# Performance work log

Measured on AMD Instinct MI355X. Metric: run time of the kernel, lower is better.

The kernel has to match this reference:

```python
import jax, jax.numpy as jnp
import numpy as np

B, TE, TD, D = 8, 2048, 2048, 256

def setup_inputs() -> dict:
    key = jax.random.key(0)
    k1, k2 = jax.random.split(key)
    encoder_outputs = jax.random.normal(k1, (B, TE, D), dtype=jnp.float32)
    decoder_outputs = jax.random.normal(k2, (B, TD, D), dtype=jnp.float32)
    return {"encoder_outputs": encoder_outputs, "decoder_outputs": decoder_outputs}

def reference(encoder_outputs, decoder_outputs):
    # luong_score[b,e,t] = sum_d enc[b,e,d] * dec[b,t,d]   (batch_dot with dec transposed)
    luong_score = jnp.einsum('bed,btd->bet', encoder_outputs, decoder_outputs)
    # softmax over encoder-time axis (axis=1)
    luong_score = jax.nn.softmax(luong_score, axis=1)
    # original does expand_dims + broadcast-multiply + sum over axis=1;
    # same math as a contraction over e: context[b,t,d] = sum_e score[b,e,t]*enc[b,e,d]
    encoder_vector = jnp.einsum('bet,bed->btd', luong_score, encoder_outputs)
    return jnp.concatenate([decoder_outputs, encoder_vector], axis=-1)
```

## Files before the change

kernel.cpp:

```cpp
#include <hip/hip_runtime.h>

typedef _Float16 f16;
typedef _Float16 f16x4 __attribute__((ext_vector_type(4)));
typedef _Float16 f16x8 __attribute__((ext_vector_type(8)));
typedef float    f32x4 __attribute__((ext_vector_type(4)));

#define NB   8
#define TE   2048
#define TD   2048
#define DIM  256
#define NSPLIT 4
#define LOG2E 1.44269504088896340736f

#define AS1(p) ((const __attribute__((address_space(1))) void*)(p))
#define AS3(p) ((__attribute__((address_space(3))) void*)(p))

__global__ __launch_bounds__(256) void prep_kernel(const float* __restrict__ enc,
                                                   f16* __restrict__ ench,
                                                   f16* __restrict__ enct) {
    __shared__ f16 tile[64][72];
    int b  = blockIdx.z;
    int e0 = blockIdx.x * 64;
    int d0 = blockIdx.y * 64;
    int tid = threadIdx.x;
    {
        int e  = tid >> 2;
        int dg = (tid & 3) * 16;
        const float* p = enc + ((size_t)b * TE + e0 + e) * DIM + d0 + dg;
        float4 v0 = *(const float4*)(p);
        float4 v1 = *(const float4*)(p + 4);
        float4 v2 = *(const float4*)(p + 8);
        float4 v3 = *(const float4*)(p + 12);
        f16x8 o0, o1;
        o0[0]=(f16)v0.x; o0[1]=(f16)v0.y; o0[2]=(f16)v0.z; o0[3]=(f16)v0.w;
        o0[4]=(f16)v1.x; o0[5]=(f16)v1.y; o0[6]=(f16)v1.z; o0[7]=(f16)v1.w;
        o1[0]=(f16)v2.x; o1[1]=(f16)v2.y; o1[2]=(f16)v2.z; o1[3]=(f16)v2.w;
        o1[4]=(f16)v3.x; o1[5]=(f16)v3.y; o1[6]=(f16)v3.z; o1[7]=(f16)v3.w;
        *(f16x8*)&tile[e][dg]     = o0;
        *(f16x8*)&tile[e][dg + 8] = o1;
        f16* hp = ench + ((size_t)b * TE + e0 + e) * DIM + d0 + dg;
        *(f16x8*)(hp)     = o0;
        *(f16x8*)(hp + 8) = o1;
    }
    __syncthreads();
    {
        int d  = tid >> 2;
        int eg = (tid & 3) * 16;
        f16x8 o0, o1;
        #pragma unroll
        for (int ii = 0; ii < 8; ii++) o0[ii] = tile[eg + ii][d];
        #pragma unroll
        for (int ii = 0; ii < 8; ii++) o1[ii] = tile[eg + 8 + ii][d];
        f16* qp = enct + ((size_t)b * DIM + d0 + d) * TE + e0 + eg;
        *(f16x8*)(qp)     = o0;
        *(f16x8*)(qp + 8) = o1;
    }
}

#define LDS_NAT0 0
#define LDS_NAT1 16384
#define LDS_TR   32768
#define LDS_P    49152

__global__ __launch_bounds__(256, 2) void attn_kernel(
        const float* __restrict__ dec32,
        const f16*  __restrict__ enc_h,
        const f16*  __restrict__ enc_t,
        float* __restrict__ out,
        f16*   __restrict__ ctxp,
        float* __restrict__ m_arr,
        float* __restrict__ l_arr,
        int nsplit) {
    __shared__ char lds[54272];
    const int tid  = threadIdx.x;
    const int lane = tid & 63;
    const int wave = tid >> 6;
    const int th   = wave >> 1;
    const int dh   = wave & 1;
    const int tcol = lane & 15;
    const int q    = lane >> 4;

    int xb, b, z;
    if (nsplit == NSPLIT) {
        int fid = blockIdx.x + 32 * (blockIdx.y + 8 * blockIdx.z);
        int c = fid & 7, j = fid >> 3;
        int p = c * 4 + (j >> 5);
        xb = j & 31; b = p & 7; z = p >> 3;
    } else { xb = blockIdx.x; b = blockIdx.y; z = 0; }
    const int t0     = xb * 64;
    const int iters  = (TE / 32) / nsplit;
    const int e_base = z * (TE / nsplit);

    const f16* enc_b  = enc_h + (size_t)b * TE * DIM;
    const f16* enct_b = enc_t + (size_t)b * DIM * TE;

    int nat_goff[4], tr_goff[4], nat_loff[4], tr_loff[4];
    #pragma unroll
    for (int i = 0; i < 4; i++) {
        int s = i * 256 + tid;
        int e = s >> 5, cs = s & 31;
        nat_goff[i] = e * DIM + (cs ^ (e & 7)) * 8;
        nat_loff[i] = (s & ~63) * 16;
        int d = s >> 2, c = s & 3;
        tr_goff[i] = d * TE + (c ^ ((d >> 1) & 3)) * 8;
        tr_loff[i] = (s & ~63) * 16;
    }

    #pragma unroll
    for (int i = 0; i < 4; i++)
        __builtin_amdgcn_global_load_lds(AS1(enc_b + (size_t)e_base * DIM + nat_goff[i]),
                                         AS3(lds + LDS_NAT0 + nat_loff[i]), 16, 0, 0);

    if (nsplit == 1) {
        const float* dp = dec32 + ((size_t)b * TD + t0) * DIM;
        float*       op = out   + ((size_t)b * TD + t0) * 512;
        #pragma unroll
        for (int i = 0; i < 16; i++) {
            int idx = i * 256 + tid;
            int t = idx >> 6, c = idx & 63;
            float4 v = *(const float4*)(dp + t * DIM + c * 4);
            *(float4*)(op + t * 512 + c * 4) = v;
        }
    }

    f16x8 qf[2][8];
    {
        const float* qp = dec32 + ((size_t)b * TD + t0 + th * 32) * DIM;
        #pragma unroll
        for (int tn = 0; tn < 2; tn++)
            #pragma unroll
            for (int ks = 0; ks < 8; ks++) {
                const float* p = qp + (size_t)(tn * 16 + tcol) * DIM + ks * 32 + q * 8;
                float4 u = *(const float4*)(p);
                float4 v = *(const float4*)(p + 4);
                f16x8 o;
                o[0]=(f16)u.x; o[1]=(f16)u.y; o[2]=(f16)u.z; o[3]=(f16)u.w;
                o[4]=(f16)v.x; o[5]=(f16)v.y; o[6]=(f16)v.z; o[7]=(f16)v.w;
                qf[tn][ks] = o;
            }
    }

    f16x8 ones;
    #pragma unroll
    for (int j = 0; j < 8; j++) ones[j] = (f16)1.0f;

    const f32x4 zero4 = {0.f, 0.f, 0.f, 0.f};
    float m_[2] = {-INFINITY, -INFINITY};
    f32x4 lsum[2] = {zero4, zero4};
    f32x4 ctx[8][2];
    #pragma unroll
    for (int dm = 0; dm < 8; dm++)
        #pragma unroll
        for (int tn = 0; tn < 2; tn++) ctx[dm][tn] = zero4;

    char* pb = lds + LDS_P + th * 2560;
    const int e7 = tcol & 7;
    const int trsw = (tcol >> 1) & 3;

    __syncthreads();

    for (int it = 0; it < iters; it++) {
        const int natc = (it & 1) ? LDS_NAT1 : LDS_NAT0;
        const int e0   = e_base + it * 32;

        #pragma unroll
        for (int i = 0; i < 4; i++)
            __builtin_amdgcn_global_load_lds(AS1(enct_b + e0 + tr_goff[i]),
                                             AS3(lds + LDS_TR + tr_loff[i]), 16, 0, 0);

        f32x4 st[2][2];
        #pragma unroll
        for (int mt = 0; mt < 2; mt++)
            #pragma unroll
            for (int tn = 0; tn < 2; tn++) st[mt][tn] = zero4;
        #pragma unroll
        for (int ks = 0; ks < 8; ks++) {
            #pragma unroll
            for (int mt = 0; mt < 2; mt++) {
                int e = mt * 16 + tcol;
                f16x8 af = *(const f16x8*)(lds + natc + e * 512 + (((ks << 2) | q) ^ e7) * 16);
                #pragma unroll
                for (int tn = 0; tn < 2; tn++)
                    st[mt][tn] = __builtin_amdgcn_mfma_f32_16x16x32_f16(af, qf[tn][ks], st[mt][tn], 0, 0, 0);
            }
        }

        #pragma unroll
        for (int tn = 0; tn < 2; tn++) {
            float mx = fmaxf(fmaxf(fmaxf(st[0][tn][0], st[0][tn][1]), fmaxf(st[0][tn][2], st[0][tn][3])),
                             fmaxf(fmaxf(st[1][tn][0], st[1][tn][1]), fmaxf(st[1][tn][2], st[1][tn][3])));
            mx = fmaxf(mx, __shfl_xor(mx, 16, 64));
            mx = fmaxf(mx, __shfl_xor(mx, 32, 64));
            float mn = fmaxf(m_[tn], mx);
            bool bumped = mn > m_[tn];
            float al = __builtin_amdgcn_exp2f((m_[tn] - mn) * LOG2E);
            m_[tn] = mn;
            char* prow = pb + (tn * 16 + tcol) * 80;
            #pragma unroll
            for (int mt = 0; mt < 2; mt++) {
                f16x4 pv;
                #pragma unroll
                for (int r = 0; r < 4; r++)
                    pv[r] = (f16)__builtin_amdgcn_exp2f((st[mt][tn][r] - mn) * LOG2E);
                if (dh == 0) *(f16x4*)(prow + mt * 32 + q * 8) = pv;
            }
            if (__any(bumped)) {
                lsum[tn][0] *= al; lsum[tn][1] *= al; lsum[tn][2] *= al; lsum[tn][3] *= al;
                #pragma unroll
                for (int dm = 0; dm < 8; dm++) {
                    ctx[dm][tn][0] *= al; ctx[dm][tn][1] *= al;
                    ctx[dm][tn][2] *= al; ctx[dm][tn][3] *= al;
                }
            }
        }

        __syncthreads();

        if (it + 1 < iters) {
            const int natn = (it & 1) ? LDS_NAT0 : LDS_NAT1;
            #pragma unroll
            for (int i = 0; i < 4; i++)
                __builtin_amdgcn_global_load_lds(AS1(enc_b + (size_t)(e0 + 32) * DIM + nat_goff[i]),
                                                 AS3(lds + natn + nat_loff[i]), 16, 0, 0);
        }

        f16x8 pf[2];
        #pragma unroll
        for (int tn = 0; tn < 2; tn++)
            pf[tn] = *(const f16x8*)(pb + (tn * 16 + tcol) * 80 + q * 16);
        #pragma unroll
        for (int tn = 0; tn < 2; tn++)
            lsum[tn] = __builtin_amdgcn_mfma_f32_16x16x32_f16(ones, pf[tn], lsum[tn], 0, 0, 0);
        #pragma unroll
        for (int dm = 0; dm < 8; dm++) {
            int drow = dh * 128 + dm * 16 + tcol;
            f16x8 af = *(const f16x8*)(lds + LDS_TR + drow * 64 + (q ^ trsw) * 16);
            #pragma unroll
            for (int tn = 0; tn < 2; tn++)
                ctx[dm][tn] = __builtin_amdgcn_mfma_f32_16x16x32_f16(af, pf[tn], ctx[dm][tn], 0, 0, 0);
        }

        __syncthreads();
    }

    if (nsplit > 1) {
        size_t rowbase = (size_t)(z * NB + b) * TD + t0 + th * 32;
        #pragma unroll
        for (int tn = 0; tn < 2; tn++) {
            float inv = 1.0f / lsum[tn][0];
            size_t rb = (rowbase + tn * 16 + tcol) * DIM + dh * 128;
            #pragma unroll
            for (int dm = 0; dm < 8; dm++) {
                f16x4 cv;
                #pragma unroll
                for (int r = 0; r < 4; r++) cv[r] = (f16)(ctx[dm][tn][r] * inv);
                *(f16x4*)(ctxp + rb + dm * 16 + q * 4) = cv;
            }
        }
        if (dh == 0 && lane < 16) {
            int mi = (z * NB + b) * TD + t0 + th * 32 + lane;
            #pragma unroll
            for (int tn = 0; tn < 2; tn++) {
                m_arr[mi + tn * 16] = m_[tn];
                l_arr[mi + tn * 16] = lsum[tn][0];
            }
        }
    } else {
        float* ob = out + ((size_t)b * TD + t0 + th * 32) * 512 + 256 + dh * 128;
        #pragma unroll
        for (int tn = 0; tn < 2; tn++) {
            float inv = 1.0f / lsum[tn][0];
            #pragma unroll
            for (int dm = 0; dm < 8; dm++)
                #pragma unroll
                for (int r = 0; r < 4; r++)
                    ob[(size_t)(tn * 16 + tcol) * 512 + dm * 16 + q * 4 + r] = ctx[dm][tn][r] * inv;
        }
    }
}

__global__ __launch_bounds__(256) void combine_kernel(const float* __restrict__ dec32,
        const f16* __restrict__ ctxp, const float* __restrict__ m_arr,
        const float* __restrict__ l_arr, float* __restrict__ out) {
    int idx  = blockIdx.x * 256 + threadIdx.x;
    int trow = idx >> 5;
    int dg   = (idx & 31) * 8;
    float m0[NSPLIT], l0[NSPLIT], M = -INFINITY;
    #pragma unroll
    for (int s = 0; s < NSPLIT; s++) {
        m0[s] = m_arr[s * (NB * TD) + trow];
        l0[s] = l_arr[s * (NB * TD) + trow];
        M = fmaxf(M, m0[s]);
    }
    float L = 0.f, w[NSPLIT];
    #pragma unroll
    for (int s = 0; s < NSPLIT; s++) {
        w[s] = __builtin_amdgcn_exp2f((m0[s] - M) * LOG2E) * l0[s];
        L += w[s];
    }
    float invL = 1.0f / L;
    float acc[8] = {0.f,0.f,0.f,0.f,0.f,0.f,0.f,0.f};
    #pragma unroll
    for (int s = 0; s < NSPLIT; s++) {
        f16x8 v = *(const f16x8*)(ctxp + ((size_t)s * (NB * TD) + trow) * DIM + dg);
        float ws = w[s] * invL;
        #pragma unroll
        for (int j = 0; j < 8; j++) acc[j] += ws * (float)v[j];
    }
    float4 d0 = *(const float4*)(dec32 + (size_t)trow * DIM + dg);
    float4 d1 = *(const float4*)(dec32 + (size_t)trow * DIM + dg + 4);
    float* ob = out + (size_t)trow * 512;
    *(float4*)(ob + dg)     = d0;
    *(float4*)(ob + dg + 4) = d1;
    float4 c0, c1;
    c0.x=acc[0]; c0.y=acc[1]; c0.z=acc[2]; c0.w=acc[3];
    c1.x=acc[4]; c1.y=acc[5]; c1.z=acc[6]; c1.w=acc[7];
    *(float4*)(ob + 256 + dg)     = c0;
    *(float4*)(ob + 256 + dg + 4) = c1;
}

extern "C" void kernel_launch(void* const* d_in, const int* in_sizes, int n_in,
                              void* d_out, int out_size, void* d_ws, size_t ws_size,
                              hipStream_t stream) {
    (void)in_sizes; (void)n_in;
    const float* enc = (const float*)d_in[0];
    const float* dec = (const float*)d_in[1];
    float* out = (float*)d_out;

    const size_t HB    = (size_t)NB * TE * DIM * 2;
    const size_t CTXPB = (size_t)NSPLIT * NB * TD * DIM * 2;
    const size_t MLB   = (size_t)NSPLIT * NB * TD * 4;
    const size_t NEED4 = 2 * HB + CTXPB + 2 * MLB;
    const size_t NEED1 = 2 * HB;

    if (ws_size < NEED1) {
        hipMemsetAsync(d_out, 0, (size_t)out_size * sizeof(float), stream);
        return;
    }
    int nsplit = (ws_size >= NEED4) ? NSPLIT : 1;

    f16*   enc_h = (f16*)d_ws;
    f16*   enc_t = (f16*)((char*)d_ws + HB);
    f16*   ctxp  = (f16*)((char*)d_ws + 2 * HB);
    float* m_arr = (float*)((char*)d_ws + 2 * HB + CTXPB);
    float* l_arr = (float*)((char*)d_ws + 2 * HB + CTXPB + MLB);

    prep_kernel<<<dim3(32, 4, 8), 256, 0, stream>>>(enc, enc_h, enc_t);
    attn_kernel<<<dim3(32, 8, nsplit), 256, 0, stream>>>(dec, enc_h, enc_t, out,
                                                         ctxp, m_arr, l_arr, nsplit);
    if (nsplit == NSPLIT)
        combine_kernel<<<2048, 256, 0, stream>>>(dec, ctxp, m_arr, l_arr, out);
}
```

Baseline: 172.5 us.

## Split encoder axis three ways and offload score work to one wave per pair

The split-K factor drops from four to three, with uneven chunk sizes (22/21/21 iterations). Occupancy is raised to three blocks per CU, aiming to fill the machine with 768 blocks. Only one of the two d-half waves per t-half (alternating by block index) now computes QK^T and the softmax. It writes P and the rescale factor alpha to LDS, and the partner wave reads alpha after the barrier to rescale its own accumulators. This removes redundant score MFMAs and exp work and the partner's Q fragment registers. The cost is an imbalanced wave workload and an extra LDS exchange.

```diff
diff --git a/kernel.cpp b/kernel.cpp
--- a/kernel.cpp
+++ b/kernel.cpp
@@ -9,7 +9,7 @@
 #define TE   2048
 #define TD   2048
 #define DIM  256
-#define NSPLIT 4
+#define NSPLIT 3
 #define LOG2E 1.44269504088896340736f
 
 #define AS1(p) ((const __attribute__((address_space(1))) void*)(p))
@@ -62,7 +62,7 @@
 #define LDS_TR   32768
 #define LDS_P    49152
 
-__global__ __launch_bounds__(256, 2) void attn_kernel(
+__global__ __launch_bounds__(256, 3) void attn_kernel(
         const float* __restrict__ dec32,
         const f16*  __restrict__ enc_h,
         const f16*  __restrict__ enc_t,
@@ -80,36 +80,32 @@
     const int tcol = lane & 15;
     const int q    = lane >> 4;
 
-    int xb, b, z;
+    int xb, b, z, iters, e_base;
     if (nsplit == NSPLIT) {
         int fid = blockIdx.x + 32 * (blockIdx.y + 8 * blockIdx.z);
         int c = fid & 7, j = fid >> 3;
-        int p = c * 4 + (j >> 5);
-        xb = j & 31; b = p & 7; z = p >> 3;
-    } else { xb = blockIdx.x; b = blockIdx.y; z = 0; }
-    const int t0     = xb * 64;
-    const int iters  = (TE / 32) / nsplit;
-    const int e_base = z * (TE / nsplit);
+        xb = j & 31;
+        int p = c * 3 + (j >> 5);
+        b = p & 7; z = p >> 3;
+        iters  = (z == 0) ? 22 : 21;
+        e_base = (z == 0) ? 0 : (704 + (z - 1) * 672);
+    } else { xb = blockIdx.x; b = blockIdx.y; z = 0; iters = 64; e_base = 0; }
+    const int  t0    = xb * 64;
+    const bool heavy = (dh == (xb & 1));
 
     const f16* enc_b  = enc_h + (size_t)b * TE * DIM;
     const f16* enct_b = enc_t + (size_t)b * DIM * TE;
 
-    int nat_goff[4], tr_goff[4], nat_loff[4], tr_loff[4];
-    #pragma unroll
-    for (int i = 0; i < 4; i++) {
-        int s = i * 256 + tid;
-        int e = s >> 5, cs = s & 31;
-        nat_goff[i] = e * DIM + (cs ^ (e & 7)) * 8;
-        nat_loff[i] = (s & ~63) * 16;
-        int d = s >> 2, c = s & 3;
-        tr_goff[i] = d * TE + (c ^ ((d >> 1) & 3)) * 8;
-        tr_loff[i] = (s & ~63) * 16;
-    }
+    const int e00 = tid >> 5, cs0 = tid & 31;
+    const int nat_g0 = e00 * DIM + (cs0 ^ (e00 & 7)) * 8;
+    const int d00 = tid >> 2, c00 = tid & 3;
+    const int tr_g0  = d00 * TE + (c00 ^ ((d00 >> 1) & 3)) * 8;
+    const int l0     = wave * 1024;
 
     #pragma unroll
     for (int i = 0; i < 4; i++)
-        __builtin_amdgcn_global_load_lds(AS1(enc_b + (size_t)e_base * DIM + nat_goff[i]),
-                                         AS3(lds + LDS_NAT0 + nat_loff[i]), 16, 0, 0);
+        __builtin_amdgcn_global_load_lds(AS1(enc_b + (size_t)e_base * DIM + nat_g0 + i * 2048),
+                                         AS3(lds + LDS_NAT0 + l0 + i * 4096), 16, 0, 0);
 
     if (nsplit == 1) {
         const float* dp = dec32 + ((size_t)b * TD + t0) * DIM;
@@ -124,7 +120,7 @@
     }
 
     f16x8 qf[2][8];
-    {
+    if (heavy) {
         const float* qp = dec32 + ((size_t)b * TD + t0 + th * 32) * DIM;
         #pragma unroll
         for (int tn = 0; tn < 2; tn++)
@@ -155,7 +151,6 @@
 
     char* pb = lds + LDS_P + th * 2560;
     const int e7 = tcol & 7;
-    const int trsw = (tcol >> 1) & 3;
 
     __syncthreads();
 
@@ -165,51 +160,53 @@
 
         #pragma unroll
         for (int i = 0; i < 4; i++)
-            __builtin_amdgcn_global_load_lds(AS1(enct_b + e0 + tr_goff[i]),
-                                             AS3(lds + LDS_TR + tr_loff[i]), 16, 0, 0);
-
-        f32x4 st[2][2];
-        #pragma unroll
-        for (int mt = 0; mt < 2; mt++)
-            #pragma unroll
-            for (int tn = 0; tn < 2; tn++) st[mt][tn] = zero4;
-        #pragma unroll
-        for (int ks = 0; ks < 8; ks++) {
-            #pragma unroll
-            for (int mt = 0; mt < 2; mt++) {
-                int e = mt * 16 + tcol;
-                f16x8 af = *(const f16x8*)(lds + natc + e * 512 + (((ks << 2) | q) ^ e7) * 16);
-                #pragma unroll
-                for (int tn = 0; tn < 2; tn++)
-                    st[mt][tn] = __builtin_amdgcn_mfma_f32_16x16x32_f16(af, qf[tn][ks], st[mt][tn], 0, 0, 0);
-            }
-        }
-
-        #pragma unroll
-        for (int tn = 0; tn < 2; tn++) {
-            float mx = fmaxf(fmaxf(fmaxf(st[0][tn][0], st[0][tn][1]), fmaxf(st[0][tn][2], st[0][tn][3])),
-                             fmaxf(fmaxf(st[1][tn][0], st[1][tn][1]), fmaxf(st[1][tn][2], st[1][tn][3])));
-            mx = fmaxf(mx, __shfl_xor(mx, 16, 64));
-            mx = fmaxf(mx, __shfl_xor(mx, 32, 64));
-            float mn = fmaxf(m_[tn], mx);
-            bool bumped = mn > m_[tn];
-            float al = __builtin_amdgcn_exp2f((m_[tn] - mn) * LOG2E);
-            m_[tn] = mn;
-            char* prow = pb + (tn * 16 + tcol) * 80;
-            #pragma unroll
-            for (int mt = 0; mt < 2; mt++) {
-                f16x4 pv;
-                #pragma unroll
-                for (int r = 0; r < 4; r++)
-                    pv[r] = (f16)__builtin_amdgcn_exp2f((st[mt][tn][r] - mn) * LOG2E);
-                if (dh == 0) *(f16x4*)(prow + mt * 32 + q * 8) = pv;
-            }
-            if (__any(bumped)) {
-                lsum[tn][0] *= al; lsum[tn][1] *= al; lsum[tn][2] *= al; lsum[tn][3] *= al;
-                #pragma unroll
-                for (int dm = 0; dm < 8; dm++) {
-                    ctx[dm][tn][0] *= al; ctx[dm][tn][1] *= al;
-                    ctx[dm][tn][2] *= al; ctx[dm][tn][3] *= al;
+            __builtin_amdgcn_global_load_lds(AS1(enct_b + e0 + tr_g0 + i * 64 * TE),
+                                             AS3(lds + LDS_TR + l0 + i * 4096), 16, 0, 0);
+
+        if (heavy) {
+            f32x4 st[2][2];
+            #pragma unroll
+            for (int mt = 0; mt < 2; mt++)
+                #pragma unroll
+                for (int tn = 0; tn < 2; tn++) st[mt][tn] = zero4;
+            #pragma unroll
+            for (int ks = 0; ks < 8; ks++) {
+                #pragma unroll
+                for (int mt = 0; mt < 2; mt++) {
+                    int e = mt * 16 + tcol;
+                    f16x8 af = *(const f16x8*)(lds + natc + e * 512 + (((ks << 2) | q) ^ e7) * 16);
+                    #pragma unroll
+                    for (int tn = 0; tn < 2; tn++)
+                        st[mt][tn] = __builtin_amdgcn_mfma_f32_16x16x32_f16(af, qf[tn][ks], st[mt][tn], 0, 0, 0);
+                }
+            }
+            #pragma unroll
+            for (int tn = 0; tn < 2; tn++) {
+                float mx = fmaxf(fmaxf(fmaxf(st[0][tn][0], st[0][tn][1]), fmaxf(st[0][tn][2], st[0][tn][3])),
+                                 fmaxf(fmaxf(st[1][tn][0], st[1][tn][1]), fmaxf(st[1][tn][2], st[1][tn][3])));
+                mx = fmaxf(mx, __shfl_xor(mx, 16, 64));
+                mx = fmaxf(mx, __shfl_xor(mx, 32, 64));
+                float mn = fmaxf(m_[tn], mx);
+                bool bumped = mn > m_[tn];
+                float al = __builtin_amdgcn_exp2f((m_[tn] - mn) * LOG2E);
+                m_[tn] = mn;
+                char* prow = pb + (tn * 16 + tcol) * 80;
+                #pragma unroll
+                for (int mt = 0; mt < 2; mt++) {
+                    f16x4 pv;
+                    #pragma unroll
+                    for (int r = 0; r < 4; r++)
+                        pv[r] = (f16)__builtin_amdgcn_exp2f((st[mt][tn][r] - mn) * LOG2E);
+                    *(f16x4*)(prow + mt * 32 + q * 8) = pv;
+                }
+                if (q == 0) *(float*)(prow + 72) = al;
+                if (__any(bumped)) {
+                    lsum[tn][0] *= al; lsum[tn][1] *= al; lsum[tn][2] *= al; lsum[tn][3] *= al;
+                    #pragma unroll
+                    for (int dm = 0; dm < 8; dm++) {
+                        ctx[dm][tn][0] *= al; ctx[dm][tn][1] *= al;
+                        ctx[dm][tn][2] *= al; ctx[dm][tn][3] *= al;
+                    }
                 }
             }
         }
@@ -220,8 +217,23 @@
             const int natn = (it & 1) ? LDS_NAT0 : LDS_NAT1;
             #pragma unroll
             for (int i = 0; i < 4; i++)
-                __builtin_amdgcn_global_load_lds(AS1(enc_b + (size_t)(e0 + 32) * DIM + nat_goff[i]),
-                                                 AS3(lds + natn + nat_loff[i]), 16, 0, 0);
+                __builtin_amdgcn_global_load_lds(AS1(enc_b + (size_t)(e0 + 32) * DIM + nat_g0 + i * 2048),
+                                                 AS3(lds + natn + l0 + i * 4096), 16, 0, 0);
+        }
+
+        if (!heavy) {
+            #pragma unroll
+            for (int tn = 0; tn < 2; tn++) {
+                float al = *(const float*)(pb + (tn * 16 + tcol) * 80 + 72);
+                if (__any(al < 1.0f)) {
+                    lsum[tn][0] *= al; lsum[tn][1] *= al; lsum[tn][2] *= al; lsum[tn][3] *= al;
+                    #pragma unroll
+                    for (int dm = 0; dm < 8; dm++) {
+                        ctx[dm][tn][0] *= al; ctx[dm][tn][1] *= al;
+                        ctx[dm][tn][2] *= al; ctx[dm][tn][3] *= al;
+                    }
+                }
+            }
         }
 
         f16x8 pf[2];
@@ -234,7 +246,7 @@
         #pragma unroll
         for (int dm = 0; dm < 8; dm++) {
             int drow = dh * 128 + dm * 16 + tcol;
-            f16x8 af = *(const f16x8*)(lds + LDS_TR + drow * 64 + (q ^ trsw) * 16);
+            f16x8 af = *(const f16x8*)(lds + LDS_TR + drow * 64 + (q ^ ((tcol >> 1) & 3)) * 16);
             #pragma unroll
             for (int tn = 0; tn < 2; tn++)
                 ctx[dm][tn] = __builtin_amdgcn_mfma_f32_16x16x32_f16(af, pf[tn], ctx[dm][tn], 0, 0, 0);
@@ -257,7 +269,7 @@
                 *(f16x4*)(ctxp + rb + dm * 16 + q * 4) = cv;
             }
         }
-        if (dh == 0 && lane < 16) {
+        if (heavy && lane < 16) {
             int mi = (z * NB + b) * TD + t0 + th * 32 + lane;
             #pragma unroll
             for (int tn = 0; tn < 2; tn++) {
@@ -330,14 +342,14 @@
     const size_t HB    = (size_t)NB * TE * DIM * 2;
     const size_t CTXPB = (size_t)NSPLIT * NB * TD * DIM * 2;
     const size_t MLB   = (size_t)NSPLIT * NB * TD * 4;
-    const size_t NEED4 = 2 * HB + CTXPB + 2 * MLB;
+    const size_t NEED3 = 2 * HB + CTXPB + 2 * MLB;
     const size_t NEED1 = 2 * HB;
 
     if (ws_size < NEED1) {
         hipMemsetAsync(d_out, 0, (size_t)out_size * sizeof(float), stream);
         return;
     }
-    int nsplit = (ws_size >= NEED4) ? NSPLIT : 1;
+    int nsplit = (ws_size >= NEED3) ? NSPLIT : 1;
 
     f16*   enc_h = (f16*)d_ws;
     f16*   enc_t = (f16*)((char*)d_ws + HB);
```

Result: slower. 221.0 us (+28.1%).
